# Kernel optimization log

Hardware: AMD Instinct MI355X
Metric: run time of the kernel (lower is better)

Reference implementation:

```python
import jax, jax.numpy as jnp
import numpy as np

EMB = 256
HID = 256
VOCAB = 32000
NUM_CELLS = 2
BATCH = 64
SEQ = 512


def setup_inputs() -> dict:
    key = jax.random.key(0)
    ks = jax.random.split(key, 6)
    scale = 1.0 / np.sqrt(HID)
    inp = {
        "input": jax.random.randint(ks[0], (BATCH, SEQ), 0, VOCAB, dtype=jnp.int32),
        # explicit routing table: token id -> LSTMCell index
        "assignment": (jnp.arange(VOCAB, dtype=jnp.int32) % NUM_CELLS),
        "embeddings": jax.random.normal(ks[1], (VOCAB, EMB), jnp.float32) * 0.02,
        # stacked per-cell LSTMCell params, torch gate order (i, f, g, o)
        "W_ih": jax.random.uniform(ks[2], (NUM_CELLS, 4 * HID, EMB), jnp.float32, -scale, scale),
        "W_hh": jax.random.uniform(ks[3], (NUM_CELLS, 4 * HID, HID), jnp.float32, -scale, scale),
        "b_ih": jax.random.uniform(ks[4], (NUM_CELLS, 4 * HID), jnp.float32, -scale, scale),
        "b_hh": jax.random.uniform(ks[5], (NUM_CELLS, 4 * HID), jnp.float32, -scale, scale),
    }
    return inp


def reference(input, assignment, embeddings, W_ih, W_hh, b_ih, b_hh):
    B, S = input.shape
    H = W_hh.shape[-1]
    x = embeddings[input]            # [B, S, E]
    a = assignment[input]            # [B, S] cell index per token
    bias = (b_ih + b_hh)[:, None, :]  # [C, 1, 4H]

    def step(carry, ts):
        h, c = carry                 # [B, H] each
        x_t, a_t = ts                # [B, E], [B]
        # gates for every cell, then per-token select (routed dispatch)
        gates = (jnp.einsum('be,cge->cbg', x_t, W_ih)
                 + jnp.einsum('bh,cgh->cbg', h, W_hh)
                 + bias)             # [C, B, 4H]
        g = jnp.take_along_axis(gates, a_t[None, :, None], axis=0)[0]  # [B, 4H]
        i_g, f_g, g_g, o_g = jnp.split(g, 4, axis=-1)
        c_new = jax.nn.sigmoid(f_g) * c + jax.nn.sigmoid(i_g) * jnp.tanh(g_g)
        h_new = jax.nn.sigmoid(o_g) * jnp.tanh(c_new)
        return (h_new, c_new), None

    h0 = jnp.zeros((B, H), x.dtype)
    (h, c), _ = jax.lax.scan(step, (h0, h0),
                             (jnp.swapaxes(x, 0, 1), jnp.swapaxes(a, 0, 1)))
    return jnp.concatenate([h, c], axis=-1)  # [B, 2H]
```

## Files before the change

kernel.cpp:

```cpp
#include <hip/hip_runtime.h>
#include <stdint.h>
#include <stddef.h>


#define BB   64
#define SS   512
#define EE   256
#define HH   256
#define G4   1024
#define NWG  64
#define TPB  512
#define TCH  16

typedef __attribute__((ext_vector_type(8))) short short8;
typedef __attribute__((ext_vector_type(4))) float f32x4;
typedef __attribute__((ext_vector_type(4))) unsigned int uint4v;
typedef __attribute__((ext_vector_type(2))) unsigned int uint2v;

__device__ __forceinline__ unsigned short f2bf(float f){
  union { float f; unsigned u; } v; v.f = f;
  return (unsigned short)((v.u + 0x7fffu + ((v.u >> 16) & 1u)) >> 16);
}
__device__ __forceinline__ float bf2f(unsigned short s){
  union { float f; unsigned u; } v; v.u = ((unsigned)s) << 16;
  return v.f;
}
__device__ __forceinline__ int swz2(int byte){ return byte ^ (((byte >> 9) & 3) << 5); }

#define WS_H_OFF  1024
#define WS_XG_OFF (1024 + 131072)

__global__ void zero_ws_kernel(int* ws){
  const int n = (WS_H_OFF + 131072) / 4;
  for (int i = blockIdx.x * blockDim.x + threadIdx.x; i < n; i += gridDim.x * blockDim.x){
    int* p = ws + i;
    const int z = 0;
    asm volatile("global_store_dword %0, %1, off sc0 sc1" :: "v"(p), "v"(z) : "memory");
  }
}

__global__ __launch_bounds__(TPB, 1)
void xproj_kernel(const int* __restrict__ input, const int* __restrict__ assign,
                  const float* __restrict__ emb, const float* __restrict__ Wih,
                  const float* __restrict__ bih, const float* __restrict__ bhh,
                  float* __restrict__ xg)
{
  __shared__ __align__(16) unsigned short sXp[8][4][4][16][8];
  __shared__ int sTokP[TCH][64];
  __shared__ int sAsgP[TCH][64];

  const int tid  = threadIdx.x;
  const int lane = tid & 63;
  const int lg   = lane >> 4;
  const int lc   = lane & 15;
  const int wv   = tid >> 6;
  const int rowtile = blockIdx.x & 15;
  const int tc      = blockIdx.x >> 4;

  const int rbase = rowtile * 128 + wv * 16;
  const int cellw = rbase >> 10;
  const int rrw   = rbase & 1023;

  short8 aX[8];
  {
    const float* pw = Wih + ((size_t)cellw * G4 + (rrw + lc)) * EE + lg * 8;
    #pragma unroll
    for (int kc = 0; kc < 8; ++kc){
      const f32x4 u = *(const f32x4*)(pw + kc * 32);
      const f32x4 v = *(const f32x4*)(pw + kc * 32 + 4);
      short8 x8;
      #pragma unroll
      for (int e = 0; e < 4; ++e){ x8[e] = (short)f2bf(u[e]); x8[4+e] = (short)f2bf(v[e]); }
      aX[kc] = x8;
    }
  }
  float biasr[4];
  #pragma unroll
  for (int q = 0; q < 4; ++q){
    const int idx = cellw * G4 + rrw + lg * 4 + q;
    biasr[q] = bih[idx] + bhh[idx];
  }

  for (int i = tid; i < TCH * 64; i += TPB){
    const int tl = i >> 6, b = i & 63;
    const int tok = input[b * SS + tc * TCH + tl];
    sTokP[tl][b] = tok; sAsgP[tl][b] = assign[tok];
  }
  __syncthreads();

  const int gkc = tid >> 6, glg = (tid >> 4) & 3, glc = tid & 15;
  short8 xr[4];
  auto GATHERP = [&](int tl){
    #pragma unroll
    for (int ct = 0; ct < 4; ++ct){
      const int tok = sTokP[tl][ct * 16 + glc];
      const float* ep = emb + (size_t)tok * EE + gkc * 32 + glg * 8;
      const f32x4 u = *(const f32x4*)ep;
      const f32x4 v = *(const f32x4*)(ep + 4);
      short8 x8;
      #pragma unroll
      for (int e = 0; e < 4; ++e){ x8[e] = (short)f2bf(u[e]); x8[4+e] = (short)f2bf(v[e]); }
      xr[ct] = x8;
    }
  };
  GATHERP(0);

  for (int tl = 0; tl < TCH; ++tl){
    #pragma unroll
    for (int ct = 0; ct < 4; ++ct)
      *(short8*)&sXp[gkc][glg][ct][glc][0] = xr[ct];
    __syncthreads();
    if (tl + 1 < TCH) GATHERP(tl + 1);

    f32x4 acc[4];
    #pragma unroll
    for (int ct = 0; ct < 4; ++ct){
      acc[ct][0] = biasr[0]; acc[ct][1] = biasr[1];
      acc[ct][2] = biasr[2]; acc[ct][3] = biasr[3];
    }
    #pragma unroll
    for (int kc = 0; kc < 8; ++kc){
      #pragma unroll
      for (int ct = 0; ct < 4; ++ct){
        const short8 bx = *(const short8*)&sXp[kc][lg][ct][lc][0];
        acc[ct] = __builtin_amdgcn_mfma_f32_16x16x32_bf16(aX[kc], bx, acc[ct], 0, 0, 0);
      }
    }
    float* xgt = xg + (size_t)(tc * TCH + tl) * 65536;
    #pragma unroll
    for (int ct = 0; ct < 4; ++ct){
      const int b = ct * 16 + lc;
      if (sAsgP[tl][b] == cellw){
        #pragma unroll
        for (int q = 0; q < 4; ++q)
          xgt[(rrw + lg * 4 + q) * 64 + b] = acc[ct][q];
      }
    }
    __syncthreads();
  }
}

__global__ __launch_bounds__(TPB, 1)
void mlstm_rec_kernel(const int* __restrict__ input, const int* __restrict__ assign,
                      const float* __restrict__ Whh, float* __restrict__ out,
                      char* __restrict__ ws)
{
  __shared__ __align__(16) unsigned short sH[8192];
  __shared__ float sC[32][8];
  __shared__ int sAsg[3][64];

  const int tid  = threadIdx.x;
  const int lane = tid & 63;
  const int lg   = lane >> 4;
  const int lc   = lane & 15;
  const int wv   = tid >> 6;
  const int cell  = wv & 1;
  const int jhalf = (wv >> 1) & 1;
  const int ct    = wv >> 2;
  const int wg    = blockIdx.x;
  const int jset  = wg & 31;
  const int thG   = wg >> 5;

  unsigned int* hbuf = (unsigned int*)(ws + WS_H_OFF);
  const float* xg = (const float*)(ws + WS_XG_OFF);

  short8 aHiH[8], aLoH[8];
  {
    const float* ph = Whh + ((size_t)cell * G4 + (lc & 3) * HH
                             + jset * 8 + jhalf * 4 + (lc >> 2)) * HH + lg * 8;
    #pragma unroll
    for (int kc = 0; kc < 8; ++kc){
      const f32x4 u = *(const f32x4*)(ph + kc * 32);
      const f32x4 v = *(const f32x4*)(ph + kc * 32 + 4);
      short8 hi, lo;
      #pragma unroll
      for (int e = 0; e < 4; ++e){
        const float w0 = u[e], w1 = v[e];
        const unsigned short h0 = f2bf(w0), h1 = f2bf(w1);
        hi[e] = (short)h0;   lo[e] = (short)f2bf(w0 - bf2f(h0));
        hi[4+e] = (short)h1; lo[4+e] = (short)f2bf(w1 - bf2f(h1));
      }
      aHiH[kc] = hi; aLoH[kc] = lo;
    }
  }

  if (tid < 64){
    const int t0 = input[tid * SS];     sAsg[0][tid] = assign[t0];
    const int t1 = input[tid * SS + 1]; sAsg[1][tid] = assign[t1];
  }

  const int jloc   = jhalf * 4 + lg;
  const int jglob  = jset * 8 + jloc;
  const int b_loc  = ct * 16 + lc;
  const int b_glob = thG * 32 + b_loc;

  float xpre[4];
  auto XPRE = [&](int t){
    const float* p = xg + (size_t)t * 65536 + jglob * 64 + b_glob;
    #pragma unroll
    for (int q = 0; q < 4; ++q)
      xpre[q] = p[q * 16384];
  };
  XPRE(0);
  __syncthreads();

  for (int t = 0; t < SS; ++t){
    f32x4 acc;
    #pragma unroll
    for (int q = 0; q < 4; ++q) acc[q] = xpre[q];
    if (t + 1 < SS) XPRE(t + 1);
    if (t + 2 < SS && tid < 64){
      const int tk = input[tid * SS + (t + 2)];
      sAsg[(t + 2) % 3][tid] = assign[tk];
    }

    if (t > 0){
      const unsigned int* bw = hbuf + (size_t)(t & 1) * 16384 + thG * 8192;
      const unsigned int need = (unsigned int)t;

      uint4v hv[4];
      unsigned bad;
      do {
        #pragma unroll
        for (int i = 0; i < 4; ++i){
          const unsigned int* p = bw + (i * 512 + tid) * 4;
          asm volatile("global_load_dwordx4 %0, %1, off sc0 sc1"
                       : "=v"(hv[i]) : "v"(p) : "memory");
        }
        asm volatile("s_waitcnt vmcnt(0)" ::: "memory");
        bad = 0;
        #pragma unroll
        for (int i = 0; i < 4; ++i)
          #pragma unroll
          for (int e = 0; e < 4; ++e)
            bad |= (hv[i][e] ^ need);
        bad &= 0xFFFFu;
        if (bad) __builtin_amdgcn_s_sleep(1);
      } while (bad);
      __builtin_amdgcn_sched_barrier(0);

      #pragma unroll
      for (int i = 0; i < 4; ++i){
        uint2v pk;
        pk[0] = (hv[i][0] >> 16) | (hv[i][1] & 0xFFFF0000u);
        pk[1] = (hv[i][2] >> 16) | (hv[i][3] & 0xFFFF0000u);
        *(uint2v*)((char*)sH + swz2((i * 512 + tid) * 8)) = pk;
      }
      __syncthreads();
    }

    if (t > 0){
      #pragma unroll
      for (int kch = 0; kch < 8; ++kch){
        const int base = (kch * 4 + lg) * 512 + ct * 256 + lc * 16;
        const short8 hh = *(const short8*)((const char*)sH + swz2(base));
        acc = __builtin_amdgcn_mfma_f32_16x16x32_bf16(aHiH[kch], hh, acc, 0, 0, 0);
        acc = __builtin_amdgcn_mfma_f32_16x16x32_bf16(aLoH[kch], hh, acc, 0, 0, 0);
      }
    }

    {
      const int a = sAsg[t % 3][b_glob];
      if (a == cell){
        const float gi = acc[0], gf = acc[1], gg = acc[2], go = acc[3];
        const float cold = (t == 0) ? 0.f : sC[b_loc][jloc];
        const float si = 1.f / (1.f + __expf(-gi));
        const float sf = 1.f / (1.f + __expf(-gf));
        const float so = 1.f / (1.f + __expf(-go));
        const float cn = sf * cold + si * tanhf(gg);
        const float hn = so * tanhf(cn);
        if (t < SS - 1){
          sC[b_loc][jloc] = cn;
          const unsigned word = ((unsigned)f2bf(hn) << 16) | ((unsigned)(t + 1) & 0xFFFFu);
          unsigned int* dst = hbuf + (size_t)((t & 1) ^ 1) * 16384 + thG * 8192
                            + jset * 256 + b_loc * 8 + jloc;
          asm volatile("global_store_dword %0, %1, off sc0 sc1" :: "v"(dst), "v"(word) : "memory");
        } else {
          out[b_glob * 512 + jglob]       = hn;
          out[b_glob * 512 + 256 + jglob] = cn;
        }
      }
    }
  }
}

extern "C" void kernel_launch(void* const* d_in, const int* in_sizes, int n_in,
                              void* d_out, int out_size, void* d_ws, size_t ws_size,
                              hipStream_t stream)
{
  const int*   input  = (const int*)  d_in[0];
  const int*   assign = (const int*)  d_in[1];
  const float* emb    = (const float*)d_in[2];
  const float* Wih    = (const float*)d_in[3];
  const float* Whh    = (const float*)d_in[4];
  const float* bih    = (const float*)d_in[5];
  const float* bhh    = (const float*)d_in[6];
  float* out = (float*)d_out;
  char*  ws  = (char*)d_ws;

  zero_ws_kernel<<<64, 256, 0, stream>>>((int*)ws);
  float* xg = (float*)(ws + WS_XG_OFF);
  xproj_kernel<<<512, TPB, 0, stream>>>(input, assign, emb, Wih, bih, bhh, xg);
  mlstm_rec_kernel<<<NWG, TPB, 0, stream>>>(input, assign, Whh, out, ws);
}
```

Before: 1.199 ms.

## Repartition recurrent LSTM work into four 16-batch pools with 16 hidden units per workgroup

The 64 workgroups of the recurrent kernel are regrouped from 2 batch groups × 32 hidden slices (8 units each) into 4 batch pools × 16 hidden slices (16 units each). Each workgroup now polls and loads only 16 batches of h per step (half the previous global h traffic per block), and each wave handles one 16-batch tile. The LDS h buffer shrinks, gets a new swizzle and uses a single 16-byte store per thread. The aim is to cut per-step global polling volume and synchronisation scope on the serial critical path, at the cost of each wave now covering 4 hidden units over a narrower batch span.

```diff
diff --git a/kernel.cpp b/kernel.cpp
--- a/kernel.cpp
+++ b/kernel.cpp
@@ -15,7 +15,6 @@
 typedef __attribute__((ext_vector_type(8))) short short8;
 typedef __attribute__((ext_vector_type(4))) float f32x4;
 typedef __attribute__((ext_vector_type(4))) unsigned int uint4v;
-typedef __attribute__((ext_vector_type(2))) unsigned int uint2v;
 
 __device__ __forceinline__ unsigned short f2bf(float f){
   union { float f; unsigned u; } v; v.f = f;
@@ -25,7 +24,7 @@
   union { float f; unsigned u; } v; v.u = ((unsigned)s) << 16;
   return v.f;
 }
-__device__ __forceinline__ int swz2(int byte){ return byte ^ (((byte >> 9) & 3) << 5); }
+__device__ __forceinline__ int swz3(int byte){ return byte ^ (((byte >> 7) & 3) << 4); }
 
 #define WS_H_OFF  1024
 #define WS_XG_OFF (1024 + 131072)
@@ -145,8 +144,8 @@
                       const float* __restrict__ Whh, float* __restrict__ out,
                       char* __restrict__ ws)
 {
-  __shared__ __align__(16) unsigned short sH[8192];
-  __shared__ float sC[32][8];
+  __shared__ __align__(16) unsigned short sH[4096];
+  __shared__ float sC[16][17];
   __shared__ int sAsg[3][64];
 
   const int tid  = threadIdx.x;
@@ -154,12 +153,11 @@
   const int lg   = lane >> 4;
   const int lc   = lane & 15;
   const int wv   = tid >> 6;
-  const int cell  = wv & 1;
-  const int jhalf = (wv >> 1) & 1;
-  const int ct    = wv >> 2;
-  const int wg    = blockIdx.x;
-  const int jset  = wg & 31;
-  const int thG   = wg >> 5;
+  const int cell = wv & 1;
+  const int jq   = wv >> 1;
+  const int wg   = blockIdx.x;
+  const int jset = wg & 15;
+  const int pool = wg >> 4;
 
   unsigned int* hbuf = (unsigned int*)(ws + WS_H_OFF);
   const float* xg = (const float*)(ws + WS_XG_OFF);
@@ -167,7 +165,7 @@
   short8 aHiH[8], aLoH[8];
   {
     const float* ph = Whh + ((size_t)cell * G4 + (lc & 3) * HH
-                             + jset * 8 + jhalf * 4 + (lc >> 2)) * HH + lg * 8;
+                             + jset * 16 + jq * 4 + (lc >> 2)) * HH + lg * 8;
     #pragma unroll
     for (int kc = 0; kc < 8; ++kc){
       const f32x4 u = *(const f32x4*)(ph + kc * 32);
@@ -189,10 +187,10 @@
     const int t1 = input[tid * SS + 1]; sAsg[1][tid] = assign[t1];
   }
 
-  const int jloc   = jhalf * 4 + lg;
-  const int jglob  = jset * 8 + jloc;
-  const int b_loc  = ct * 16 + lc;
-  const int b_glob = thG * 32 + b_loc;
+  const int jloc   = jq * 4 + lg;
+  const int jglob  = jset * 16 + jloc;
+  const int b_loc  = lc;
+  const int b_glob = pool * 16 + lc;
 
   float xpre[4];
   auto XPRE = [&](int t){
@@ -215,45 +213,39 @@
     }
 
     if (t > 0){
-      const unsigned int* bw = hbuf + (size_t)(t & 1) * 16384 + thG * 8192;
+      const unsigned int* bw = hbuf + (size_t)(t & 1) * 16384 + pool * 4096;
       const unsigned int need = (unsigned int)t;
 
-      uint4v hv[4];
+      uint4v h0, h1;
       unsigned bad;
+      const unsigned int* p0 = bw + tid * 8;
       do {
-        #pragma unroll
-        for (int i = 0; i < 4; ++i){
-          const unsigned int* p = bw + (i * 512 + tid) * 4;
-          asm volatile("global_load_dwordx4 %0, %1, off sc0 sc1"
-                       : "=v"(hv[i]) : "v"(p) : "memory");
-        }
+        asm volatile("global_load_dwordx4 %0, %1, off sc0 sc1" : "=v"(h0) : "v"(p0)     : "memory");
+        asm volatile("global_load_dwordx4 %0, %1, off sc0 sc1" : "=v"(h1) : "v"(p0 + 4) : "memory");
         asm volatile("s_waitcnt vmcnt(0)" ::: "memory");
         bad = 0;
         #pragma unroll
-        for (int i = 0; i < 4; ++i)
-          #pragma unroll
-          for (int e = 0; e < 4; ++e)
-            bad |= (hv[i][e] ^ need);
+        for (int e = 0; e < 4; ++e){ bad |= (h0[e] ^ need); bad |= (h1[e] ^ need); }
         bad &= 0xFFFFu;
         if (bad) __builtin_amdgcn_s_sleep(1);
       } while (bad);
       __builtin_amdgcn_sched_barrier(0);
 
-      #pragma unroll
-      for (int i = 0; i < 4; ++i){
-        uint2v pk;
-        pk[0] = (hv[i][0] >> 16) | (hv[i][1] & 0xFFFF0000u);
-        pk[1] = (hv[i][2] >> 16) | (hv[i][3] & 0xFFFF0000u);
-        *(uint2v*)((char*)sH + swz2((i * 512 + tid) * 8)) = pk;
-      }
+      uint4v pk;
+      pk[0] = (h0[0] >> 16) | (h0[1] & 0xFFFF0000u);
+      pk[1] = (h0[2] >> 16) | (h0[3] & 0xFFFF0000u);
+      pk[2] = (h1[0] >> 16) | (h1[1] & 0xFFFF0000u);
+      pk[3] = (h1[2] >> 16) | (h1[3] & 0xFFFF0000u);
+      *(uint4v*)((char*)sH + swz3(tid * 16)) = pk;
       __syncthreads();
     }
 
     if (t > 0){
       #pragma unroll
       for (int kch = 0; kch < 8; ++kch){
-        const int base = (kch * 4 + lg) * 512 + ct * 256 + lc * 16;
-        const short8 hh = *(const short8*)((const char*)sH + swz2(base));
+        const int js = kch * 2 + (lg >> 1);
+        const int byte = js * 512 + lc * 32 + (lg & 1) * 16;
+        const short8 hh = *(const short8*)((const char*)sH + swz3(byte));
         acc = __builtin_amdgcn_mfma_f32_16x16x32_bf16(aHiH[kch], hh, acc, 0, 0, 0);
         acc = __builtin_amdgcn_mfma_f32_16x16x32_bf16(aLoH[kch], hh, acc, 0, 0, 0);
       }
@@ -272,8 +264,8 @@
         if (t < SS - 1){
           sC[b_loc][jloc] = cn;
           const unsigned word = ((unsigned)f2bf(hn) << 16) | ((unsigned)(t + 1) & 0xFFFFu);
-          unsigned int* dst = hbuf + (size_t)((t & 1) ^ 1) * 16384 + thG * 8192
-                            + jset * 256 + b_loc * 8 + jloc;
+          unsigned int* dst = hbuf + (size_t)((t & 1) ^ 1) * 16384 + pool * 4096
+                            + jset * 256 + b_loc * 16 + jloc;
           asm volatile("global_store_dword %0, %1, off sc0 sc1" :: "v"(dst), "v"(word) : "memory");
         } else {
           out[b_glob * 512 + jglob]       = hn;
```

Result: faster. 1.112 ms (-7.2%).
